# Kernel optimization log

Hardware: AMD Instinct MI355X
Metric: run time of the kernel (lower is better)

## Reference

```python
import jax, jax.numpy as jnp
import numpy as np

EMBED_DIM = 1024
NUM_HEADS = 16
HEAD_DIM = EMBED_DIM // NUM_HEADS
B, SQ, SK = 4, 2048, 2048


def setup_inputs() -> dict:
    key = jax.random.key(0)
    ks = jax.random.split(key, 8)
    d = EMBED_DIM
    # xavier-uniform-like scale for projection weights
    lim = float(np.sqrt(6.0 / (d + d)))
    def w(k):
        return jax.random.uniform(k, (d, d), jnp.float32, -lim, lim)
    return {
        "q": jax.random.normal(ks[0], (B, SQ, d), jnp.float32),
        "k": jax.random.normal(ks[1], (B, SK, d), jnp.float32),
        "v": jax.random.normal(ks[2], (B, SK, d), jnp.float32),
        "Wq": w(ks[3]), "bq": jnp.zeros((d,), jnp.float32),
        "Wk": w(ks[4]), "bk": jnp.zeros((d,), jnp.float32),
        "Wv": w(ks[5]), "bv": jnp.zeros((d,), jnp.float32),
        "Wo": w(ks[6]), "bo": jnp.zeros((d,), jnp.float32),
    }


def reference(q, k, v, Wq, bq, Wk, bk, Wv, bv, Wo, bo):
    # nn.Linear applies x @ W.T + b
    Bq = q.shape[0]
    scale = HEAD_DIM ** (-0.5)
    def split_heads(x):  # [B, S, D] -> [B, H, S, Hd]
        return x.reshape(Bq, -1, NUM_HEADS, HEAD_DIM).transpose(0, 2, 1, 3)
    _q = split_heads(q @ Wq.T + bq)
    _k = split_heads(k @ Wk.T + bk)
    _v = split_heads(v @ Wv.T + bv)
    attn = jnp.einsum("bhqd,bhkd->bhqk", _q, _k) * scale
    attn = jax.nn.softmax(attn, axis=-1)
    x = jnp.einsum("bhqk,bhkd->bhqd", attn, _v)
    x = x.transpose(0, 2, 1, 3).reshape(Bq, -1, EMBED_DIM)
    x = x @ Wo.T + bo
    return (x, attn)
```

## Files before the change

### kernel.cpp

```cpp
#include <hip/hip_runtime.h>
#include <hip/hip_bf16.h>


typedef _Float16 h4 __attribute__((ext_vector_type(4)));
typedef _Float16 h8 __attribute__((ext_vector_type(8)));
typedef float f4 __attribute__((ext_vector_type(4)));

#define EMBED 1024
#define HEADS 16
#define HD 64
#define BB 4
#define SS 2048
#define MROWS (BB * SS)

#define GLD(src, dst)                                                                  \
  __builtin_amdgcn_global_load_lds((const __attribute__((address_space(1))) void*)(src), \
                                   (__attribute__((address_space(3))) void*)(dst), 16, 0, 0)

__device__ inline float fexp2(float x) {
  float r;
  asm("v_exp_f32 %0, %1" : "=v"(r) : "v"(x));
  return r;
}

__global__ __launch_bounds__(256) void cast3_f32_f16(const float* __restrict__ a,
                                                     const float* __restrict__ b,
                                                     const float* __restrict__ c,
                                                     _Float16* __restrict__ oa,
                                                     _Float16* __restrict__ ob,
                                                     _Float16* __restrict__ oc, int n) {
  const float* in = blockIdx.y == 0 ? a : blockIdx.y == 1 ? b : c;
  _Float16* out = blockIdx.y == 0 ? oa : blockIdx.y == 1 ? ob : oc;
  int i = (blockIdx.x * 256 + threadIdx.x) * 4;
  if (i < n) {
    float4 v = *reinterpret_cast<const float4*>(in + i);
    h4 o = {(_Float16)v.x, (_Float16)v.y, (_Float16)v.z, (_Float16)v.w};
    *reinterpret_cast<h4*>(out + i) = o;
  }
}

__global__ __launch_bounds__(256) void cast4_f32_f16(const float* __restrict__ a,
                                                     const float* __restrict__ b,
                                                     const float* __restrict__ c,
                                                     const float* __restrict__ d,
                                                     _Float16* __restrict__ oa,
                                                     _Float16* __restrict__ ob,
                                                     _Float16* __restrict__ oc,
                                                     _Float16* __restrict__ od, int n) {
  const float* in = blockIdx.y == 0 ? a : blockIdx.y == 1 ? b : blockIdx.y == 2 ? c : d;
  _Float16* out = blockIdx.y == 0 ? oa : blockIdx.y == 1 ? ob : blockIdx.y == 2 ? oc : od;
  int i = (blockIdx.x * 256 + threadIdx.x) * 4;
  if (i < n) {
    float4 v = *reinterpret_cast<const float4*>(in + i);
    h4 o = {(_Float16)v.x, (_Float16)v.y, (_Float16)v.z, (_Float16)v.w};
    *reinterpret_cast<h4*>(out + i) = o;
  }
}

template <int OUTF32>
__device__ __forceinline__ void gemm_body(const _Float16* __restrict__ A,
                                          const _Float16* __restrict__ W,
                                          const float* __restrict__ bias,
                                          void* __restrict__ out, char* smem) {
  char* la = smem;
  char* lb = smem + 16384;
  const int t = threadIdx.x;
  const int lane = t & 63;
  const int w = t >> 6;
  const int g = lane >> 4, r16 = lane & 15;
  const int wr = (w >> 1) * 64, wc = (w & 1) * 64;
  const int m0 = blockIdx.x * 128, n0 = blockIdx.y * 128;
  const int p_in_wave = (w << 10) + (lane << 4);

  const char* Ab = (const char*)A;
  const char* Wb = (const char*)W;

  f4 acc[4][4] = {};

  for (int kt = 0; kt < EMBED; kt += 64) {
#pragma unroll
    for (int c = 0; c < 4; c++) {
      int p0 = c * 4096 + p_in_wave;
      int row = p0 >> 7;
      int scol = (p0 & 127) ^ ((row & 7) << 4);
      GLD(Ab + ((size_t)(m0 + row) * EMBED + kt) * 2 + scol, la + c * 4096 + (w << 10));
      GLD(Wb + ((size_t)(n0 + row) * EMBED + kt) * 2 + scol, lb + c * 4096 + (w << 10));
    }
    __syncthreads();
    const int sw = (r16 & 7) << 4;
#pragma unroll
    for (int kk = 0; kk < 2; kk++) {
      h8 af[4], bf[4];
#pragma unroll
      for (int m = 0; m < 4; m++)
        af[m] = *(const h8*)(la + (wr + m * 16 + r16) * 128 + ((kk * 64 + 16 * g) ^ sw));
#pragma unroll
      for (int n = 0; n < 4; n++)
        bf[n] = *(const h8*)(lb + (wc + n * 16 + r16) * 128 + ((kk * 64 + 16 * g) ^ sw));
#pragma unroll
      for (int m = 0; m < 4; m++)
#pragma unroll
        for (int n = 0; n < 4; n++)
          acc[m][n] = __builtin_amdgcn_mfma_f32_16x16x32_f16(af[m], bf[n], acc[m][n], 0, 0, 0);
    }
    __syncthreads();
  }

#pragma unroll
  for (int n = 0; n < 4; n++) {
    int gc = n0 + wc + n * 16 + r16;
    float bv = bias[gc];
#pragma unroll
    for (int m = 0; m < 4; m++) {
#pragma unroll
      for (int r = 0; r < 4; r++) {
        int gr = m0 + wr + m * 16 + 4 * g + r;
        float vv = acc[m][n][r] + bv;
        if (OUTF32)
          reinterpret_cast<float*>(out)[(size_t)gr * EMBED + gc] = vv;
        else
          reinterpret_cast<_Float16*>(out)[(size_t)gr * EMBED + gc] = (_Float16)vv;
      }
    }
  }
}

__global__ __launch_bounds__(256, 2) void gemm_qkv(const _Float16* qh, const _Float16* kh,
                                                   const _Float16* vh, const _Float16* wq,
                                                   const _Float16* wk, const _Float16* wv,
                                                   const float* bq, const float* bk,
                                                   const float* bv, _Float16* Q, _Float16* K,
                                                   _Float16* V) {
  __shared__ char smem[32768];
  const int z = blockIdx.z;
  const _Float16* A = z == 0 ? qh : z == 1 ? kh : vh;
  const _Float16* W = z == 0 ? wq : z == 1 ? wk : wv;
  const float* bias = z == 0 ? bq : z == 1 ? bk : bv;
  _Float16* out = z == 0 ? Q : z == 1 ? K : V;
  gemm_body<0>(A, W, bias, (void*)out, smem);
}

__global__ __launch_bounds__(256, 2) void gemm_out(const _Float16* __restrict__ A,
                                                   const _Float16* __restrict__ W,
                                                   const float* __restrict__ bias,
                                                   float* __restrict__ out) {
  __shared__ char smem[32768];
  gemm_body<1>(A, W, bias, (void*)out, smem);
}

__global__ __launch_bounds__(256) void transpose_v(const _Float16* __restrict__ Vp,
                                                   _Float16* __restrict__ Vt) {
  __shared__ _Float16 tile[64][72];
  const int s0 = blockIdx.x * 64;
  const int bh = blockIdx.y;
  const int b = bh >> 4, h = bh & 15;
  const int t = threadIdx.x;
#pragma unroll
  for (int it = 0; it < 2; it++) {
    int c = t + it * 256;
    int r = c >> 3, c8 = (c & 7) * 8;
    *reinterpret_cast<float4*>(&tile[r][c8]) =
        *reinterpret_cast<const float4*>(Vp + ((size_t)b * SS + s0 + r) * EMBED + h * HD + c8);
  }
  __syncthreads();
#pragma unroll
  for (int it = 0; it < 2; it++) {
    int c = t + it * 256;
    int d = c >> 3, s8 = (c & 7) * 8;
    int s32 = s8 & 31;
    int hf = s32 >> 4;
    int g0 = (s32 & 8) ? 2 : 0;
    h4 lo = {tile[s8 + 0][d], tile[s8 + 1][d], tile[s8 + 2][d], tile[s8 + 3][d]};
    h4 hi = {tile[s8 + 4][d], tile[s8 + 5][d], tile[s8 + 6][d], tile[s8 + 7][d]};
    _Float16* base = Vt + ((size_t)bh * HD + d) * SS + s0 + (s8 & ~31);
    *reinterpret_cast<h4*>(base + g0 * 8 + hf * 4) = lo;
    *reinterpret_cast<h4*>(base + (g0 + 1) * 8 + hf * 4) = hi;
  }
}

__global__ __launch_bounds__(256, 2) void attn_fused(const _Float16* __restrict__ Q,
                                                     const _Float16* __restrict__ K,
                                                     const _Float16* __restrict__ Vt,
                                                     float* __restrict__ attn_out,
                                                     _Float16* __restrict__ Oh) {
  __shared__ char smem[32768];
  const int t = threadIdx.x;
  const int lane = t & 63;
  const int w = t >> 6;
  const int g = lane >> 4, r16 = lane & 15;
  const int qt = blockIdx.x;
  const int bh = blockIdx.y;
  const int b = bh >> 4, h = bh & 15;
  const int qrow = qt * 64 + w * 16 + r16;
  const int p_in_wave = (w << 10) + (lane << 4);
  const int sw = (r16 & 7) << 4;

  const float CC = 0.1803368801f;

  const char* kbase = (const char*)K + ((size_t)b * SS * EMBED + h * HD) * 2;
  const char* vtbase = (const char*)Vt + (size_t)bh * HD * SS * 2;

  int srow[2], scol[2];
#pragma unroll
  for (int c = 0; c < 2; c++) {
    int p0 = c * 4096 + p_in_wave;
    srow[c] = p0 >> 7;
    scol[c] = (p0 & 127) ^ ((srow[c] & 7) << 4);
  }

#define STAGE_K(boff, kb)                                                              \
  {                                                                                    \
    _Pragma("unroll") for (int c = 0; c < 2; c++)                                      \
        GLD(kbase + (size_t)((kb) * 64 + srow[c]) * 2048 + scol[c],                    \
            smem + (boff) + c * 4096 + (w << 10));                                     \
  }
#define STAGE_V(boff, kb)                                                              \
  {                                                                                    \
    _Pragma("unroll") for (int c = 0; c < 2; c++)                                      \
        GLD(vtbase + (size_t)srow[c] * 4096 + (kb) * 128 + scol[c],                    \
            smem + (boff) + c * 4096 + (w << 10));                                     \
  }

  h8 qf[2];
  const _Float16* qptr = Q + ((size_t)b * SS + qrow) * EMBED + h * HD;
#pragma unroll
  for (int kk = 0; kk < 2; kk++)
    qf[kk] = *reinterpret_cast<const h8*>(qptr + kk * 32 + 8 * g);

  float l_run = 0.0f;
  STAGE_K(0, 0);
  __syncthreads();
  for (int kb = 0; kb < 32; kb++) {
    const char* cur = smem + (kb & 1) * 8192;
    if (kb < 31) STAGE_K(((kb + 1) & 1) * 8192, kb + 1);
    float s = 0.f;
    __builtin_amdgcn_s_setprio(1);
#pragma unroll
    for (int kf = 0; kf < 4; kf++) {
      f4 sf = {0.f, 0.f, 0.f, 0.f};
#pragma unroll
      for (int kk = 0; kk < 2; kk++) {
        h8 af = *(const h8*)(cur + (kf * 16 + r16) * 128 + ((kk * 64 + 16 * g) ^ sw));
        sf = __builtin_amdgcn_mfma_f32_16x16x32_f16(af, qf[kk], sf, 0, 0, 0);
      }
#pragma unroll
      for (int r = 0; r < 4; r++) s += fexp2(sf[r] * CC);
    }
    __builtin_amdgcn_s_setprio(0);
    s += __shfl_xor(s, 16, 64);
    s += __shfl_xor(s, 32, 64);
    l_run += s;
    __syncthreads();
  }
  const float lgr = -__log2f(l_run);

  f4 oacc[4] = {};
  float* arow = attn_out + ((size_t)bh * SS + qrow) * SS;

  STAGE_K(0, 0);
  STAGE_V(16384, 0);
  __syncthreads();
  for (int kb = 0; kb < 32; kb++) {
    const char* ck = smem + (kb & 1) * 8192;
    const char* cv = smem + 16384 + (kb & 1) * 8192;
    if (kb < 31) {
      STAGE_K(((kb + 1) & 1) * 8192, kb + 1);
      STAGE_V(16384 + ((kb + 1) & 1) * 8192, kb + 1);
    }
    h4 pa[4];
    __builtin_amdgcn_s_setprio(1);
#pragma unroll
    for (int kf = 0; kf < 4; kf++) {
      f4 sf = {0.f, 0.f, 0.f, 0.f};
#pragma unroll
      for (int kk = 0; kk < 2; kk++) {
        h8 af = *(const h8*)(ck + (kf * 16 + r16) * 128 + ((kk * 64 + 16 * g) ^ sw));
        sf = __builtin_amdgcn_mfma_f32_16x16x32_f16(af, qf[kk], sf, 0, 0, 0);
      }
      __builtin_amdgcn_s_setprio(0);
      float a0 = fexp2(fmaf(sf[0], CC, lgr));
      float a1 = fexp2(fmaf(sf[1], CC, lgr));
      float a2 = fexp2(fmaf(sf[2], CC, lgr));
      float a3 = fexp2(fmaf(sf[3], CC, lgr));
      f4 st = {a0, a1, a2, a3};
      __builtin_nontemporal_store(st, reinterpret_cast<f4*>(arow + kb * 64 + kf * 16 + 4 * g));
      pa[kf] = h4{(_Float16)a0, (_Float16)a1, (_Float16)a2, (_Float16)a3};
      __builtin_amdgcn_s_setprio(1);
    }
#pragma unroll
    for (int kf2 = 0; kf2 < 2; kf2++) {
      h8 pa8 = __builtin_shufflevector(pa[2 * kf2], pa[2 * kf2 + 1], 0, 1, 2, 3, 4, 5, 6, 7);
#pragma unroll
      for (int dt = 0; dt < 4; dt++) {
        h8 bf8 = *(const h8*)(cv + (dt * 16 + r16) * 128 + ((kf2 * 64 + 16 * g) ^ sw));
        oacc[dt] = __builtin_amdgcn_mfma_f32_16x16x32_f16(pa8, bf8, oacc[dt], 0, 0, 0);
      }
    }
    __builtin_amdgcn_s_setprio(0);
    __syncthreads();
  }

  const int orow0 = qt * 64 + w * 16;
#pragma unroll
  for (int dt = 0; dt < 4; dt++) {
#pragma unroll
    for (int r = 0; r < 4; r++) {
      Oh[((size_t)b * SS + orow0 + 4 * g + r) * EMBED + h * HD + dt * 16 + r16] =
          (_Float16)oacc[dt][r];
    }
  }
#undef STAGE_K
#undef STAGE_V
}

extern "C" void kernel_launch(void* const* d_in, const int* in_sizes, int n_in,
                              void* d_out, int out_size, void* d_ws, size_t ws_size,
                              hipStream_t stream) {
  const float* q  = (const float*)d_in[0];
  const float* k  = (const float*)d_in[1];
  const float* v  = (const float*)d_in[2];
  const float* Wq = (const float*)d_in[3];
  const float* bq = (const float*)d_in[4];
  const float* Wk = (const float*)d_in[5];
  const float* bk = (const float*)d_in[6];
  const float* Wv = (const float*)d_in[7];
  const float* bv = (const float*)d_in[8];
  const float* Wo = (const float*)d_in[9];
  const float* bo = (const float*)d_in[10];

  const size_t NW = (size_t)EMBED * EMBED;
  const size_t NX = (size_t)MROWS * EMBED;

  if (ws_size < (4 * NW + 6 * NX) * sizeof(_Float16)) return;
  _Float16* ws  = (_Float16*)d_ws;
  _Float16* wqh = ws;
  _Float16* wkh = wqh + NW;
  _Float16* wvh = wkh + NW;
  _Float16* woh = wvh + NW;
  _Float16* qh  = woh + NW;
  _Float16* kh  = qh + NX;
  _Float16* vh  = kh + NX;
  _Float16* Qh  = vh + NX;
  _Float16* Kh  = Qh + NX;
  _Float16* Vph = Kh + NX;
  _Float16* Vt2 = qh;
  _Float16* OhA = kh;

  float* xout = (float*)d_out;
  float* attn = xout + NX;

  cast3_f32_f16<<<dim3((NX / 4 + 255) / 256, 3), dim3(256), 0, stream>>>(q, k, v, qh, kh, vh,
                                                                         (int)NX);
  cast4_f32_f16<<<dim3((NW / 4 + 255) / 256, 4), dim3(256), 0, stream>>>(
      Wq, Wk, Wv, Wo, wqh, wkh, wvh, woh, (int)NW);

  dim3 ggrid(MROWS / 128, EMBED / 128), gblk(256);
  gemm_qkv<<<dim3(MROWS / 128, EMBED / 128, 3), gblk, 0, stream>>>(qh, kh, vh, wqh, wkh, wvh,
                                                                   bq, bk, bv, Qh, Kh, Vph);

  transpose_v<<<dim3(SS / 64, BB * HEADS), dim3(256), 0, stream>>>(Vph, Vt2);

  attn_fused<<<dim3(SS / 64, BB * HEADS), dim3(256), 0, stream>>>(Qh, Kh, Vt2, attn, OhA);

  gemm_out<<<ggrid, gblk, 0, stream>>>(OhA, woh, bo, xout);
}
```

Before: 507.8 us.

## Drop LDS staging in attention kernel; load K/V fragments directly from global

Removes the double-buffered LDS staging of K and V tiles and the per-iteration block barriers. Each lane now loads its MFMA operand fragments straight from global memory and relies on L1/L2 for reuse across the four waves. With no shared memory in use, launch bounds are raised to allow four blocks per CU. Blocks are also remapped so that neighbouring block IDs cover different heads and share query tiles, which changes L2 locality. The cost is more global/L1 traffic and exposed load latency that was previously hidden by the prefetch.

```diff
diff --git a/kernel.cpp b/kernel.cpp
--- a/kernel.cpp
+++ b/kernel.cpp
@@ -178,105 +178,74 @@
   }
 }
 
-__global__ __launch_bounds__(256, 2) void attn_fused(const _Float16* __restrict__ Q,
+__global__ __launch_bounds__(256, 4) void attn_fused(const _Float16* __restrict__ Q,
                                                      const _Float16* __restrict__ K,
                                                      const _Float16* __restrict__ Vt,
                                                      float* __restrict__ attn_out,
                                                      _Float16* __restrict__ Oh) {
-  __shared__ char smem[32768];
   const int t = threadIdx.x;
   const int lane = t & 63;
   const int w = t >> 6;
   const int g = lane >> 4, r16 = lane & 15;
-  const int qt = blockIdx.x;
-  const int bh = blockIdx.y;
+
+  const int flat = blockIdx.x + 32 * blockIdx.y;
+  const int c8 = flat & 7;
+  const int idx = flat >> 3;
+  const int bh = c8 + 8 * (idx & 7);
+  const int qt = idx >> 3;
   const int b = bh >> 4, h = bh & 15;
   const int qrow = qt * 64 + w * 16 + r16;
-  const int p_in_wave = (w << 10) + (lane << 4);
-  const int sw = (r16 & 7) << 4;
 
   const float CC = 0.1803368801f;
 
   const char* kbase = (const char*)K + ((size_t)b * SS * EMBED + h * HD) * 2;
   const char* vtbase = (const char*)Vt + (size_t)bh * HD * SS * 2;
 
-  int srow[2], scol[2];
-#pragma unroll
-  for (int c = 0; c < 2; c++) {
-    int p0 = c * 4096 + p_in_wave;
-    srow[c] = p0 >> 7;
-    scol[c] = (p0 & 127) ^ ((srow[c] & 7) << 4);
-  }
-
-#define STAGE_K(boff, kb)                                                              \
-  {                                                                                    \
-    _Pragma("unroll") for (int c = 0; c < 2; c++)                                      \
-        GLD(kbase + (size_t)((kb) * 64 + srow[c]) * 2048 + scol[c],                    \
-            smem + (boff) + c * 4096 + (w << 10));                                     \
-  }
-#define STAGE_V(boff, kb)                                                              \
-  {                                                                                    \
-    _Pragma("unroll") for (int c = 0; c < 2; c++)                                      \
-        GLD(vtbase + (size_t)srow[c] * 4096 + (kb) * 128 + scol[c],                    \
-            smem + (boff) + c * 4096 + (w << 10));                                     \
-  }
-
   h8 qf[2];
   const _Float16* qptr = Q + ((size_t)b * SS + qrow) * EMBED + h * HD;
 #pragma unroll
   for (int kk = 0; kk < 2; kk++)
     qf[kk] = *reinterpret_cast<const h8*>(qptr + kk * 32 + 8 * g);
 
+  const char* krow = kbase + (size_t)r16 * 2048 + 16 * g;
+
   float l_run = 0.0f;
-  STAGE_K(0, 0);
-  __syncthreads();
   for (int kb = 0; kb < 32; kb++) {
-    const char* cur = smem + (kb & 1) * 8192;
-    if (kb < 31) STAGE_K(((kb + 1) & 1) * 8192, kb + 1);
+    const char* kblk = krow + (size_t)kb * 64 * 2048;
     float s = 0.f;
-    __builtin_amdgcn_s_setprio(1);
 #pragma unroll
     for (int kf = 0; kf < 4; kf++) {
+      h8 af0 = *(const h8*)(kblk + (size_t)(kf * 16) * 2048);
+      h8 af1 = *(const h8*)(kblk + (size_t)(kf * 16) * 2048 + 64);
+      __builtin_amdgcn_s_setprio(1);
       f4 sf = {0.f, 0.f, 0.f, 0.f};
-#pragma unroll
-      for (int kk = 0; kk < 2; kk++) {
-        h8 af = *(const h8*)(cur + (kf * 16 + r16) * 128 + ((kk * 64 + 16 * g) ^ sw));
-        sf = __builtin_amdgcn_mfma_f32_16x16x32_f16(af, qf[kk], sf, 0, 0, 0);
-      }
+      sf = __builtin_amdgcn_mfma_f32_16x16x32_f16(af0, qf[0], sf, 0, 0, 0);
+      sf = __builtin_amdgcn_mfma_f32_16x16x32_f16(af1, qf[1], sf, 0, 0, 0);
+      __builtin_amdgcn_s_setprio(0);
 #pragma unroll
       for (int r = 0; r < 4; r++) s += fexp2(sf[r] * CC);
     }
-    __builtin_amdgcn_s_setprio(0);
     s += __shfl_xor(s, 16, 64);
     s += __shfl_xor(s, 32, 64);
     l_run += s;
-    __syncthreads();
   }
   const float lgr = -__log2f(l_run);
 
   f4 oacc[4] = {};
   float* arow = attn_out + ((size_t)bh * SS + qrow) * SS;
-
-  STAGE_K(0, 0);
-  STAGE_V(16384, 0);
-  __syncthreads();
+  const char* vrow = vtbase + (size_t)r16 * 4096 + 16 * g;
+
   for (int kb = 0; kb < 32; kb++) {
-    const char* ck = smem + (kb & 1) * 8192;
-    const char* cv = smem + 16384 + (kb & 1) * 8192;
-    if (kb < 31) {
-      STAGE_K(((kb + 1) & 1) * 8192, kb + 1);
-      STAGE_V(16384 + ((kb + 1) & 1) * 8192, kb + 1);
-    }
+    const char* kblk = krow + (size_t)kb * 64 * 2048;
     h4 pa[4];
-    __builtin_amdgcn_s_setprio(1);
 #pragma unroll
     for (int kf = 0; kf < 4; kf++) {
+      h8 af0 = *(const h8*)(kblk + (size_t)(kf * 16) * 2048);
+      h8 af1 = *(const h8*)(kblk + (size_t)(kf * 16) * 2048 + 64);
+      __builtin_amdgcn_s_setprio(1);
       f4 sf = {0.f, 0.f, 0.f, 0.f};
-#pragma unroll
-      for (int kk = 0; kk < 2; kk++) {
-        h8 af = *(const h8*)(ck + (kf * 16 + r16) * 128 + ((kk * 64 + 16 * g) ^ sw));
-        sf = __builtin_amdgcn_mfma_f32_16x16x32_f16(af, qf[kk], sf, 0, 0, 0);
-      }
+      sf = __builtin_amdgcn_mfma_f32_16x16x32_f16(af0, qf[0], sf, 0, 0, 0);
+      sf = __builtin_amdgcn_mfma_f32_16x16x32_f16(af1, qf[1], sf, 0, 0, 0);
       __builtin_amdgcn_s_setprio(0);
       float a0 = fexp2(fmaf(sf[0], CC, lgr));
       float a1 = fexp2(fmaf(sf[1], CC, lgr));
@@ -285,19 +254,18 @@
       f4 st = {a0, a1, a2, a3};
       __builtin_nontemporal_store(st, reinterpret_cast<f4*>(arow + kb * 64 + kf * 16 + 4 * g));
       pa[kf] = h4{(_Float16)a0, (_Float16)a1, (_Float16)a2, (_Float16)a3};
-      __builtin_amdgcn_s_setprio(1);
     }
 #pragma unroll
     for (int kf2 = 0; kf2 < 2; kf2++) {
       h8 pa8 = __builtin_shufflevector(pa[2 * kf2], pa[2 * kf2 + 1], 0, 1, 2, 3, 4, 5, 6, 7);
 #pragma unroll
       for (int dt = 0; dt < 4; dt++) {
-        h8 bf8 = *(const h8*)(cv + (dt * 16 + r16) * 128 + ((kf2 * 64 + 16 * g) ^ sw));
+        h8 bf8 = *(const h8*)(vrow + (size_t)(dt * 16) * 4096 + kb * 128 + kf2 * 64);
+        __builtin_amdgcn_s_setprio(1);
         oacc[dt] = __builtin_amdgcn_mfma_f32_16x16x32_f16(pa8, bf8, oacc[dt], 0, 0, 0);
+        __builtin_amdgcn_s_setprio(0);
       }
     }
-    __builtin_amdgcn_s_setprio(0);
-    __syncthreads();
   }
 
   const int orow0 = qt * 64 + w * 16;
@@ -309,8 +277,6 @@
           (_Float16)oacc[dt][r];
     }
   }
-#undef STAGE_K
-#undef STAGE_V
 }
 
 extern "C" void kernel_launch(void* const* d_in, const int* in_sizes, int n_in,
```

Measured after the change: 819.4 us. 1.61x slower.

## Split attention work across waves by key columns instead of query rows

Applied to the files above, without the earlier changes.

Each wave now owns a 16-key slice of every 64-key block and handles all 64 query rows, holding Q fragments for four query tiles. It loads one K fragment pair per block instead of eight LDS reads. Row sums are combined across waves through LDS, and the partial outputs of the four waves are reduced in LDS before the f16 store. The aim is to cut LDS reads of K and V per wave. In exchange it raises register pressure (16 output accumulators, 8 Q fragments), adds a cross-wave reduction, uses the smaller 16x16x16 MFMA for P·V, and changes the attention store pattern.

```diff
diff --git a/kernel.cpp b/kernel.cpp
--- a/kernel.cpp
+++ b/kernel.cpp
@@ -188,10 +188,10 @@
   const int lane = t & 63;
   const int w = t >> 6;
   const int g = lane >> 4, r16 = lane & 15;
-  const int qt = blockIdx.x;
+  const int qt0 = blockIdx.x;
   const int bh = blockIdx.y;
   const int b = bh >> 4, h = bh & 15;
-  const int qrow = qt * 64 + w * 16 + r16;
+  const int q0 = qt0 * 64;
   const int p_in_wave = (w << 10) + (lane << 4);
   const int sw = (r16 & 7) << 4;
 
@@ -221,41 +221,60 @@
             smem + (boff) + c * 4096 + (w << 10));                                     \
   }
 
-  h8 qf[2];
-  const _Float16* qptr = Q + ((size_t)b * SS + qrow) * EMBED + h * HD;
-#pragma unroll
-  for (int kk = 0; kk < 2; kk++)
-    qf[kk] = *reinterpret_cast<const h8*>(qptr + kk * 32 + 8 * g);
-
-  float l_run = 0.0f;
+  h8 qf[4][2];
+#pragma unroll
+  for (int qt = 0; qt < 4; qt++) {
+    const _Float16* qptr = Q + ((size_t)b * SS + q0 + qt * 16 + r16) * EMBED + h * HD;
+#pragma unroll
+    for (int kk = 0; kk < 2; kk++)
+      qf[qt][kk] = *reinterpret_cast<const h8*>(qptr + kk * 32 + 8 * g);
+  }
+
+  const int krowoff = (w * 16 + r16) * 128;
+
+  float s4[4] = {0.f, 0.f, 0.f, 0.f};
   STAGE_K(0, 0);
   __syncthreads();
   for (int kb = 0; kb < 32; kb++) {
     const char* cur = smem + (kb & 1) * 8192;
     if (kb < 31) STAGE_K(((kb + 1) & 1) * 8192, kb + 1);
-    float s = 0.f;
+    h8 af0 = *(const h8*)(cur + krowoff + ((16 * g) ^ sw));
+    h8 af1 = *(const h8*)(cur + krowoff + ((64 + 16 * g) ^ sw));
     __builtin_amdgcn_s_setprio(1);
 #pragma unroll
-    for (int kf = 0; kf < 4; kf++) {
+    for (int qt = 0; qt < 4; qt++) {
       f4 sf = {0.f, 0.f, 0.f, 0.f};
-#pragma unroll
-      for (int kk = 0; kk < 2; kk++) {
-        h8 af = *(const h8*)(cur + (kf * 16 + r16) * 128 + ((kk * 64 + 16 * g) ^ sw));
-        sf = __builtin_amdgcn_mfma_f32_16x16x32_f16(af, qf[kk], sf, 0, 0, 0);
-      }
-#pragma unroll
-      for (int r = 0; r < 4; r++) s += fexp2(sf[r] * CC);
+      sf = __builtin_amdgcn_mfma_f32_16x16x32_f16(af0, qf[qt][0], sf, 0, 0, 0);
+      sf = __builtin_amdgcn_mfma_f32_16x16x32_f16(af1, qf[qt][1], sf, 0, 0, 0);
+      __builtin_amdgcn_s_setprio(0);
+#pragma unroll
+      for (int r = 0; r < 4; r++) s4[qt] += fexp2(sf[r] * CC);
+      __builtin_amdgcn_s_setprio(1);
     }
     __builtin_amdgcn_s_setprio(0);
-    s += __shfl_xor(s, 16, 64);
-    s += __shfl_xor(s, 32, 64);
-    l_run += s;
     __syncthreads();
   }
-  const float lgr = -__log2f(l_run);
-
-  f4 oacc[4] = {};
-  float* arow = attn_out + ((size_t)bh * SS + qrow) * SS;
+#pragma unroll
+  for (int qt = 0; qt < 4; qt++) {
+    s4[qt] += __shfl_xor(s4[qt], 16, 64);
+    s4[qt] += __shfl_xor(s4[qt], 32, 64);
+  }
+  float* lds_l = (float*)smem;
+  if (lane < 16) {
+#pragma unroll
+    for (int qt = 0; qt < 4; qt++) lds_l[w * 64 + qt * 16 + lane] = s4[qt];
+  }
+  __syncthreads();
+  float lgr[4];
+#pragma unroll
+  for (int qt = 0; qt < 4; qt++) {
+    int qi = qt * 16 + r16;
+    lgr[qt] = -__log2f(lds_l[qi] + lds_l[64 + qi] + lds_l[128 + qi] + lds_l[192 + qi]);
+  }
+  __syncthreads();
+
+  f4 oacc[4][4] = {};
+  const int voff = ((w >> 1) * 64 + g * 16 + (w & 1) * 8) ^ sw;
 
   STAGE_K(0, 0);
   STAGE_V(16384, 0);
@@ -267,47 +286,75 @@
       STAGE_K(((kb + 1) & 1) * 8192, kb + 1);
       STAGE_V(16384 + ((kb + 1) & 1) * 8192, kb + 1);
     }
+    h8 af0 = *(const h8*)(ck + krowoff + ((16 * g) ^ sw));
+    h8 af1 = *(const h8*)(ck + krowoff + ((64 + 16 * g) ^ sw));
     h4 pa[4];
     __builtin_amdgcn_s_setprio(1);
 #pragma unroll
-    for (int kf = 0; kf < 4; kf++) {
+    for (int qt = 0; qt < 4; qt++) {
       f4 sf = {0.f, 0.f, 0.f, 0.f};
-#pragma unroll
-      for (int kk = 0; kk < 2; kk++) {
-        h8 af = *(const h8*)(ck + (kf * 16 + r16) * 128 + ((kk * 64 + 16 * g) ^ sw));
-        sf = __builtin_amdgcn_mfma_f32_16x16x32_f16(af, qf[kk], sf, 0, 0, 0);
-      }
+      sf = __builtin_amdgcn_mfma_f32_16x16x32_f16(af0, qf[qt][0], sf, 0, 0, 0);
+      sf = __builtin_amdgcn_mfma_f32_16x16x32_f16(af1, qf[qt][1], sf, 0, 0, 0);
       __builtin_amdgcn_s_setprio(0);
-      float a0 = fexp2(fmaf(sf[0], CC, lgr));
-      float a1 = fexp2(fmaf(sf[1], CC, lgr));
-      float a2 = fexp2(fmaf(sf[2], CC, lgr));
-      float a3 = fexp2(fmaf(sf[3], CC, lgr));
+      float a0 = fexp2(fmaf(sf[0], CC, lgr[qt]));
+      float a1 = fexp2(fmaf(sf[1], CC, lgr[qt]));
+      float a2 = fexp2(fmaf(sf[2], CC, lgr[qt]));
+      float a3 = fexp2(fmaf(sf[3], CC, lgr[qt]));
       f4 st = {a0, a1, a2, a3};
-      __builtin_nontemporal_store(st, reinterpret_cast<f4*>(arow + kb * 64 + kf * 16 + 4 * g));
-      pa[kf] = h4{(_Float16)a0, (_Float16)a1, (_Float16)a2, (_Float16)a3};
+      __builtin_nontemporal_store(
+          st, reinterpret_cast<f4*>(attn_out + ((size_t)bh * SS + q0 + qt * 16 + r16) * SS +
+                                    kb * 64 + w * 16 + 4 * g));
+      pa[qt] = h4{(_Float16)a0, (_Float16)a1, (_Float16)a2, (_Float16)a3};
       __builtin_amdgcn_s_setprio(1);
     }
 #pragma unroll
-    for (int kf2 = 0; kf2 < 2; kf2++) {
-      h8 pa8 = __builtin_shufflevector(pa[2 * kf2], pa[2 * kf2 + 1], 0, 1, 2, 3, 4, 5, 6, 7);
-#pragma unroll
-      for (int dt = 0; dt < 4; dt++) {
-        h8 bf8 = *(const h8*)(cv + (dt * 16 + r16) * 128 + ((kf2 * 64 + 16 * g) ^ sw));
-        oacc[dt] = __builtin_amdgcn_mfma_f32_16x16x32_f16(pa8, bf8, oacc[dt], 0, 0, 0);
-      }
+    for (int dt = 0; dt < 4; dt++) {
+      h4 vf = *(const h4*)(cv + (dt * 16 + r16) * 128 + voff);
+#pragma unroll
+      for (int qt = 0; qt < 4; qt++)
+        oacc[qt][dt] = __builtin_amdgcn_mfma_f32_16x16x16f16(pa[qt], vf, oacc[qt][dt], 0, 0, 0);
     }
     __builtin_amdgcn_s_setprio(0);
     __syncthreads();
   }
 
-  const int orow0 = qt * 64 + w * 16;
-#pragma unroll
-  for (int dt = 0; dt < 4; dt++) {
-#pragma unroll
-    for (int r = 0; r < 4; r++) {
-      Oh[((size_t)b * SS + orow0 + 4 * g + r) * EMBED + h * HD + dt * 16 + r16] =
-          (_Float16)oacc[dt][r];
-    }
+  float* ro = (float*)(smem + (w & 1) * 16384);
+  if (w < 2) {
+#pragma unroll
+    for (int qt = 0; qt < 4; qt++)
+#pragma unroll
+      for (int dt = 0; dt < 4; dt++)
+#pragma unroll
+        for (int r = 0; r < 4; r++)
+          ro[(qt * 16 + 4 * g + r) * 64 + dt * 16 + r16] = oacc[qt][dt][r];
+  }
+  __syncthreads();
+  if (w >= 2) {
+#pragma unroll
+    for (int qt = 0; qt < 4; qt++)
+#pragma unroll
+      for (int dt = 0; dt < 4; dt++)
+#pragma unroll
+        for (int r = 0; r < 4; r++) {
+          int a = (qt * 16 + 4 * g + r) * 64 + dt * 16 + r16;
+          ro[a] += oacc[qt][dt][r];
+        }
+  }
+  __syncthreads();
+  {
+    const float* r0 = (const float*)smem;
+    const float* r1 = (const float*)(smem + 16384);
+    int q = t >> 2, d0 = (t & 3) * 16;
+    _Float16* orow = Oh + ((size_t)b * SS + q0 + q) * EMBED + h * HD + d0;
+    h8 o0, o1;
+#pragma unroll
+    for (int i = 0; i < 8; i++)
+      o0[i] = (_Float16)(r0[q * 64 + d0 + i] + r1[q * 64 + d0 + i]);
+#pragma unroll
+    for (int i = 0; i < 8; i++)
+      o1[i] = (_Float16)(r0[q * 64 + d0 + 8 + i] + r1[q * 64 + d0 + 8 + i]);
+    *reinterpret_cast<h8*>(orow) = o0;
+    *reinterpret_cast<h8*>(orow + 8) = o1;
   }
 #undef STAGE_K
 #undef STAGE_V
```

New measurement: 465.1 us. 1.09x faster.
